# Performance work log

Measured on AMD Instinct MI355X. Metric: run time of the kernel, lower is better.

## Reference

```python
import jax, jax.numpy as jnp
import numpy as np

GROUPS = 8
EPS = 1e-5


def group_norm_dim1(x, gamma, beta):
    # Faithful to torch: GroupNorm treats dim 1 (height) as the channel axis.
    B, H, W, C = x.shape
    xg = x.reshape(B, GROUPS, H // GROUPS, W, C)
    mean = xg.mean(axis=(2, 3, 4), keepdims=True)
    var = xg.var(axis=(2, 3, 4), keepdims=True)
    xn = ((xg - mean) * jax.lax.rsqrt(var + EPS)).reshape(B, H, W, C)
    return xn * gamma[None, :, None, None] + beta[None, :, None, None]


def setup_inputs() -> dict:
    key = jax.random.key(0)
    ks = jax.random.split(key, 8)
    B, H, W, C = 4, 64, 64, 64  # height must equal units for GroupNorm to apply
    s = 1.0 / np.sqrt(C)
    return {
        "x": jax.random.normal(ks[0], (B, H, W, C), dtype=jnp.float32),
        "gamma": jnp.ones((C,), jnp.float32),
        "beta": jnp.zeros((C,), jnp.float32),
        "Wq": jax.random.normal(ks[1], (C, C), jnp.float32) * s,
        "bq": jnp.zeros((C,), jnp.float32),
        "Wk": jax.random.normal(ks[2], (C, C), jnp.float32) * s,
        "bk": jnp.zeros((C,), jnp.float32),
        "Wv": jax.random.normal(ks[3], (C, C), jnp.float32) * s,
        "bv": jnp.zeros((C,), jnp.float32),
        "Wo": jax.random.normal(ks[4], (C, C), jnp.float32) * s,
        "bo": jnp.zeros((C,), jnp.float32),
    }


def reference(x, gamma, beta, Wq, bq, Wk, bk, Wv, bv, Wo, bo):
    B, H, W, C = x.shape
    scale = C ** (-0.5)
    xn = group_norm_dim1(x, gamma, beta)
    q = xn @ Wq + bq
    k = xn @ Wk + bk
    v = xn @ Wv + bv
    # full spatial self-attention: scores [B, H, W, H*W]
    scores = jnp.einsum('bhwc,bijc->bhwij', q, k) * scale
    attn = jax.nn.softmax(scores.reshape(B, H, W, H * W), axis=-1)
    attn = attn.reshape(B, H, W, H, W)
    proj = jnp.einsum('bhwij,bijc->bhwc', attn, v)
    proj = proj @ Wo + bo
    return xn + proj
```

## Files before the change

### kernel.cpp

```cpp
#include <hip/hip_runtime.h>

typedef __bf16 bf16_t;
typedef bf16_t bf16x8 __attribute__((ext_vector_type(8)));
typedef bf16_t bf16x4 __attribute__((ext_vector_type(4)));
typedef short  short4v __attribute__((ext_vector_type(4)));
typedef float  f32x4  __attribute__((ext_vector_type(4)));

#define MFMA32(a, b, c) __builtin_amdgcn_mfma_f32_16x16x32_bf16(a, b, c, 0, 0, 0)
#define MFMA16(a, b, c) __builtin_amdgcn_mfma_f32_16x16x16bf16_1k(a, b, c, 0, 0, 0)

typedef __attribute__((address_space(3))) unsigned int       lds_u32;
typedef __attribute__((address_space(1))) const unsigned int glb_u32c;
#define DMA16(GP, LP) __builtin_amdgcn_global_load_lds((glb_u32c*)(const void*)(GP), \
                                                       (lds_u32*)(void*)(LP), 16, 0, 0)

__global__ __launch_bounds__(256) void gn1w_kernel(const float* __restrict__ x,
    float2* __restrict__ partials,
    const float* __restrict__ Wq, const float* __restrict__ Wk,
    const float* __restrict__ Wv, const float* __restrict__ Wo,
    bf16_t* __restrict__ Wt) {
  int blk = blockIdx.x, t = threadIdx.x;
  if (blk >= 256) {
    int idx = (blk - 256) * 256 + t;
    int wsel = idx >> 12, rem = idx & 4095;
    int c = rem >> 6, kk = rem & 63;
    const float* src = (wsel == 0) ? Wq : ((wsel == 1) ? Wk : ((wsel == 2) ? Wv : Wo));
    Wt[idx] = (bf16_t)src[kk * 64 + c];
    return;
  }
  const float4* x4 = (const float4*)x + (size_t)blk * 1024;
  float s = 0.f, sq = 0.f;
  #pragma unroll
  for (int u = 0; u < 4; ++u) {
    float4 v = x4[u * 256 + t];
    s  += v.x + v.y + v.z + v.w;
    sq += v.x * v.x + v.y * v.y + v.z * v.z + v.w * v.w;
  }
  for (int off = 32; off; off >>= 1) {
    s  += __shfl_down(s, off, 64);
    sq += __shfl_down(sq, off, 64);
  }
  __shared__ float2 ps[4];
  if ((t & 63) == 0) ps[t >> 6] = make_float2(s, sq);
  __syncthreads();
  if (t == 0) {
    float S = 0.f, Q = 0.f;
    #pragma unroll
    for (int i = 0; i < 4; ++i) { S += ps[i].x; Q += ps[i].y; }
    partials[blk] = make_float2(S, Q);
  }
}

__global__ __launch_bounds__(256) void gnqkv_kernel(
    const float* __restrict__ x, const float* __restrict__ gamma,
    const float* __restrict__ beta, const float2* __restrict__ parts,
    const bf16_t* __restrict__ Wt,
    const float* __restrict__ bq, const float* __restrict__ bk, const float* __restrict__ bv,
    bf16_t* __restrict__ xnb, bf16_t* __restrict__ qo, bf16_t* __restrict__ ko,
    bf16_t* __restrict__ vo) {
  __shared__ __align__(16) bf16_t xl[4096];
  int blk = blockIdx.x, t = threadIdx.x;
  int grp = blk >> 3;
  float S = 0.f, Q = 0.f;
  #pragma unroll
  for (int i = 0; i < 8; ++i) { float2 p = parts[grp * 8 + i]; S += p.x; Q += p.y; }
  float mean = S * (1.f / 32768.f);
  float rstd = rsqrtf(Q * (1.f / 32768.f) - mean * mean + 1e-5f);
  int h = blk & 63;
  float ga = gamma[h] * rstd;
  float be = beta[h] - mean * ga;
  {
    int r = t >> 2, col0 = (t & 3) * 16;
    const float4* x4 = (const float4*)(x + (size_t)blk * 4096 + r * 64 + col0);
    bf16x8 pk0, pk1;
    float4 v0 = x4[0], v1 = x4[1], v2 = x4[2], v3 = x4[3];
    pk0[0] = (bf16_t)(v0.x * ga + be); pk0[1] = (bf16_t)(v0.y * ga + be);
    pk0[2] = (bf16_t)(v0.z * ga + be); pk0[3] = (bf16_t)(v0.w * ga + be);
    pk0[4] = (bf16_t)(v1.x * ga + be); pk0[5] = (bf16_t)(v1.y * ga + be);
    pk0[6] = (bf16_t)(v1.z * ga + be); pk0[7] = (bf16_t)(v1.w * ga + be);
    pk1[0] = (bf16_t)(v2.x * ga + be); pk1[1] = (bf16_t)(v2.y * ga + be);
    pk1[2] = (bf16_t)(v2.z * ga + be); pk1[3] = (bf16_t)(v2.w * ga + be);
    pk1[4] = (bf16_t)(v3.x * ga + be); pk1[5] = (bf16_t)(v3.y * ga + be);
    pk1[6] = (bf16_t)(v3.z * ga + be); pk1[7] = (bf16_t)(v3.w * ga + be);
    *(bf16x8*)&xnb[(size_t)blk * 4096 + r * 64 + col0]     = pk0;
    *(bf16x8*)&xnb[(size_t)blk * 4096 + r * 64 + col0 + 8] = pk1;
    int sw = r & 7, j0 = (t & 3) * 2;
    *(bf16x8*)&xl[r * 64 + ((j0 ^ sw) << 3)]       = pk0;
    *(bf16x8*)&xl[r * 64 + (((j0 + 1) ^ sw) << 3)] = pk1;
  }
  __syncthreads();
  int w = t >> 6, lane = t & 63, quad = lane >> 4, l16 = lane & 15;
  int rl = w * 16 + l16, sw2 = rl & 7;
  bf16x8 a0 = *(const bf16x8*)&xl[rl * 64 + ((quad ^ sw2) << 3)];
  bf16x8 a1 = *(const bf16x8*)&xl[rl * 64 + (((quad + 4) ^ sw2) << 3)];
  int m0 = blk * 64 + w * 16;
  int bi = blk >> 6;
  int tile = blk & 63;
  size_t tbase = (size_t)bi * 262144 + (size_t)tile * 4096;
  f32x4 zero = {0.f, 0.f, 0.f, 0.f};
  const float QSCALE = 0.125f * 1.44269504088896340736f;
  #pragma unroll
  for (int outk = 0; outk < 3; ++outk) {
    const bf16_t* wt = Wt + outk * 4096;
    const float* bias = (outk == 0) ? bq : ((outk == 1) ? bk : bv);
    #pragma unroll
    for (int nt = 0; nt < 4; ++nt) {
      int col = nt * 16 + l16;
      bf16x8 b0 = *(const bf16x8*)&wt[col * 64 + quad * 8];
      bf16x8 b1 = *(const bf16x8*)&wt[col * 64 + 32 + quad * 8];
      f32x4 acc = MFMA32(a0, b0, zero);
      acc = MFMA32(a1, b1, acc);
      float bb = bias[col];
      if (outk == 0) {
        #pragma unroll
        for (int r = 0; r < 4; ++r) {
          int m = m0 + quad * 4 + r;
          qo[(size_t)m * 64 + col] = (bf16_t)((acc[r] + bb) * QSCALE);
        }
      } else if (outk == 1) {
        #pragma unroll
        for (int r = 0; r < 4; ++r) {
          int kk = (m0 & 63) + quad * 4 + r;
          ko[tbase + kk * 64 + ((((col >> 3) ^ (kk & 7)) << 3) | (col & 7))]
              = (bf16_t)(acc[r] + bb);
        }
      } else {
        bf16x4 pk;
        #pragma unroll
        for (int r = 0; r < 4; ++r) pk[r] = (bf16_t)(acc[r] + bb);
        int u = w * 4 + quad;
        *(bf16x4*)&vo[tbase + col * 64 + ((u ^ ((col & 7) << 1)) << 2)] = pk;
      }
    }
  }
}

__global__ __launch_bounds__(256, 2) void flash_kernel(
    const bf16_t* __restrict__ q, const bf16_t* __restrict__ k,
    const bf16_t* __restrict__ vp, bf16_t* __restrict__ Opb, float* __restrict__ ml) {
  __shared__ __align__(16) bf16_t Kb[2][8192];
  __shared__ __align__(16) bf16_t Vb[2][8192];
  int t = threadIdx.x;
  int w = t >> 6, lane = t & 63, quad = lane >> 4, l16 = lane & 15;
  int b = blockIdx.x, qb = blockIdx.y, sp = blockIdx.z;
  int q0 = qb * 128 + w * 32;

  bf16x8 qf[2][2];
  {
    const bf16_t* qp = q + ((size_t)b * 4096 + q0 + l16) * 64;
    #pragma unroll
    for (int qt = 0; qt < 2; ++qt)
      #pragma unroll
      for (int hh = 0; hh < 2; ++hh)
        qf[qt][hh] = *(const bf16x8*)&qp[qt * 1024 + hh * 32 + quad * 8];
  }
  f32x4 o[2][4];
  f32x4 zero = {0.f, 0.f, 0.f, 0.f};
  #pragma unroll
  for (int qt = 0; qt < 2; ++qt)
    #pragma unroll
    for (int ct = 0; ct < 4; ++ct) o[qt][ct] = zero;
  float rs[2] = {0.f, 0.f};

  const bf16_t* kimg = k  + (size_t)b * 262144 + (size_t)sp * 65536 + w * 2048 + lane * 8;
  const bf16_t* vimg = vp + (size_t)b * 262144 + (size_t)sp * 65536 + w * 2048 + lane * 8;

  #pragma unroll
  for (int i = 0; i < 4; ++i) {
    DMA16(kimg + i * 512, &Kb[0][w * 2048 + i * 512]);
    DMA16(vimg + i * 512, &Vb[0][w * 2048 + i * 512]);
  }
  __syncthreads();

  int swk = l16 & 7;
  int swv = (l16 & 7) << 1;

  for (int it = 0; it < 8; ++it) {
    int cur = it & 1;
    if (it < 7) {
      const bf16_t* kg = kimg + (it + 1) * 8192;
      const bf16_t* vg = vimg + (it + 1) * 8192;
      int nxt = cur ^ 1;
      #pragma unroll
      for (int i = 0; i < 4; ++i) {
        DMA16(kg + i * 512, &Kb[nxt][w * 2048 + i * 512]);
        DMA16(vg + i * 512, &Vb[nxt][w * 2048 + i * 512]);
      }
    }
    #pragma unroll
    for (int kt = 0; kt < 8; ++kt) {
      const bf16_t* Kh = &Kb[cur][(kt >> 2) * 4096];
      const bf16_t* Vh = &Vb[cur][(kt >> 2) * 4096];
      int krow = ((kt & 3) * 16 + l16) * 64;
      bf16x8 kf0 = *(const bf16x8*)&Kh[krow + ((quad ^ swk) << 3)];
      bf16x8 kf1 = *(const bf16x8*)&Kh[krow + (((quad + 4) ^ swk) << 3)];
      short4v va[4];
      #pragma unroll
      for (int ct = 0; ct < 4; ++ct)
        va[ct] = *(const short4v*)&Vh[(ct * 16 + l16) * 64 + ((((kt & 3) * 4 + quad) ^ swv) << 2)];
      #pragma unroll
      for (int qt = 0; qt < 2; ++qt) {
        f32x4 st = MFMA32(kf0, qf[qt][0], zero);
        st = MFMA32(kf1, qf[qt][1], st);
        bf16x4 pb;
        float psum = 0.f;
        #pragma unroll
        for (int r = 0; r < 4; ++r) {
          float p = __builtin_amdgcn_exp2f(st[r]);
          psum += p;
          pb[r] = (bf16_t)p;
        }
        rs[qt] += psum;
        short4v pshort = __builtin_bit_cast(short4v, pb);
        #pragma unroll
        for (int ct = 0; ct < 4; ++ct)
          o[qt][ct] = MFMA16(va[ct], pshort, o[qt][ct]);
      }
    }
    __syncthreads();
  }

  #pragma unroll
  for (int qt = 0; qt < 2; ++qt) {
    rs[qt] += __shfl_xor(rs[qt], 16, 64);
    rs[qt] += __shfl_xor(rs[qt], 32, 64);
  }
  size_t rbase = (size_t)sp * 16384 + (size_t)b * 4096 + q0;
  #pragma unroll
  for (int qt = 0; qt < 2; ++qt) {
    size_t row = rbase + qt * 16 + l16;
    if (quad == 0) ml[row] = rs[qt];
    #pragma unroll
    for (int ct = 0; ct < 4; ++ct) {
      bf16x4 pk;
      #pragma unroll
      for (int r = 0; r < 4; ++r) pk[r] = (bf16_t)o[qt][ct][r];
      *(bf16x4*)&Opb[row * 64 + ct * 16 + quad * 4] = pk;
    }
  }
}

__global__ __launch_bounds__(256) void proj_kernel(
    const bf16_t* __restrict__ Opb, const float* __restrict__ ml,
    const bf16_t* __restrict__ Wt, const float* __restrict__ bo,
    const bf16_t* __restrict__ xnb, float* __restrict__ out) {
  int t = threadIdx.x, w = t >> 6, lane = t & 63, quad = lane >> 4, l16 = lane & 15;
  int r0 = blockIdx.x * 64 + w * 16;
  float acc0[8], acc1[8];
  #pragma unroll
  for (int e = 0; e < 8; ++e) { acc0[e] = 0.f; acc1[e] = 0.f; }
  float lsum = 0.f;
  #pragma unroll
  for (int s = 0; s < 4; ++s) {
    size_t rr = (size_t)s * 16384 + r0 + l16;
    bf16x8 f0 = *(const bf16x8*)&Opb[rr * 64 + quad * 8];
    bf16x8 f1 = *(const bf16x8*)&Opb[rr * 64 + 32 + quad * 8];
    #pragma unroll
    for (int e = 0; e < 8; ++e) { acc0[e] += (float)f0[e]; acc1[e] += (float)f1[e]; }
    lsum += ml[rr];
  }
  float linv = 1.f / lsum;
  bf16x8 a0, a1;
  #pragma unroll
  for (int e = 0; e < 8; ++e) {
    a0[e] = (bf16_t)(acc0[e] * linv);
    a1[e] = (bf16_t)(acc1[e] * linv);
  }
  f32x4 zero = {0.f, 0.f, 0.f, 0.f};
  const bf16_t* wt = Wt + 3 * 4096;
  #pragma unroll
  for (int nt = 0; nt < 4; ++nt) {
    int col = nt * 16 + l16;
    bf16x8 b0 = *(const bf16x8*)&wt[col * 64 + quad * 8];
    bf16x8 b1 = *(const bf16x8*)&wt[col * 64 + 32 + quad * 8];
    f32x4 acc = MFMA32(a0, b0, zero);
    acc = MFMA32(a1, b1, acc);
    float bb = bo[col];
    #pragma unroll
    for (int r = 0; r < 4; ++r) {
      size_t m = (size_t)r0 + quad * 4 + r;
      out[m * 64 + col] = acc[r] + bb + (float)xnb[m * 64 + col];
    }
  }
}

extern "C" void kernel_launch(void* const* d_in, const int* in_sizes, int n_in,
                              void* d_out, int out_size, void* d_ws, size_t ws_size,
                              hipStream_t stream) {
  const float* x     = (const float*)d_in[0];
  const float* gamma = (const float*)d_in[1];
  const float* beta  = (const float*)d_in[2];
  const float* Wq    = (const float*)d_in[3];
  const float* bq    = (const float*)d_in[4];
  const float* Wk    = (const float*)d_in[5];
  const float* bk    = (const float*)d_in[6];
  const float* Wv    = (const float*)d_in[7];
  const float* bv    = (const float*)d_in[8];
  const float* Wo    = (const float*)d_in[9];
  const float* bo    = (const float*)d_in[10];
  float* out = (float*)d_out;

  char* ws = (char*)d_ws;
  bf16_t* xnb   = (bf16_t*)(ws + 0);
  bf16_t* qb    = (bf16_t*)(ws + (2u  << 20));
  bf16_t* kb    = (bf16_t*)(ws + (4u  << 20));
  bf16_t* vb    = (bf16_t*)(ws + (6u  << 20));
  bf16_t* Opb   = (bf16_t*)(ws + (8u  << 20));
  float*  ml    = (float*)(ws + (16u << 20));
  float2* parts = (float2*)(ws + (17u << 20));
  bf16_t* Wt    = (bf16_t*)(ws + (17u << 20) + 4096);

  hipLaunchKernelGGL(gn1w_kernel,  dim3(320),       dim3(256), 0, stream, x, parts, Wq, Wk, Wv, Wo, Wt);
  hipLaunchKernelGGL(gnqkv_kernel, dim3(256),       dim3(256), 0, stream, x, gamma, beta, parts, Wt, bq, bk, bv, xnb, qb, kb, vb);
  hipLaunchKernelGGL(flash_kernel, dim3(4, 32, 4),  dim3(256), 0, stream, qb, kb, vb, Opb, ml);
  hipLaunchKernelGGL(proj_kernel,  dim3(256),       dim3(256), 0, stream, Opb, ml, Wt, bo, xnb, out);
}
```

Baseline: 120.6 us.

## Stage QKV outputs through LDS for coalesced stores and widen V reads

The projection kernel now writes each Q and K tile into shared memory first, then copies it to global memory with contiguous 16-byte stores instead of scattered 2-byte writes. The V image layout is changed to an 8-element swizzle, which the attention kernel reads with 16-byte loads covering two key subtiles. The attention loop is reorganised so one wide V load feeds two MFMA steps. This aims to cut uncoalesced global stores and halve LDS read instructions for V, at the cost of extra barriers in the projection kernel and a layout change that both kernels must agree on.

```diff
diff --git a/kernel.cpp b/kernel.cpp
--- a/kernel.cpp
+++ b/kernel.cpp
@@ -4,6 +4,7 @@
 typedef bf16_t bf16x8 __attribute__((ext_vector_type(8)));
 typedef bf16_t bf16x4 __attribute__((ext_vector_type(4)));
 typedef short  short4v __attribute__((ext_vector_type(4)));
+typedef short  short8v __attribute__((ext_vector_type(8)));
 typedef float  f32x4  __attribute__((ext_vector_type(4)));
 
 #define MFMA32(a, b, c) __builtin_amdgcn_mfma_f32_16x16x32_bf16(a, b, c, 0, 0, 0)
@@ -93,45 +94,62 @@
   int rl = w * 16 + l16, sw2 = rl & 7;
   bf16x8 a0 = *(const bf16x8*)&xl[rl * 64 + ((quad ^ sw2) << 3)];
   bf16x8 a1 = *(const bf16x8*)&xl[rl * 64 + (((quad + 4) ^ sw2) << 3)];
+  __syncthreads();
   int m0 = blk * 64 + w * 16;
   int bi = blk >> 6;
   int tile = blk & 63;
   size_t tbase = (size_t)bi * 262144 + (size_t)tile * 4096;
   f32x4 zero = {0.f, 0.f, 0.f, 0.f};
   const float QSCALE = 0.125f * 1.44269504088896340736f;
-  #pragma unroll
-  for (int outk = 0; outk < 3; ++outk) {
-    const bf16_t* wt = Wt + outk * 4096;
-    const float* bias = (outk == 0) ? bq : ((outk == 1) ? bk : bv);
-    #pragma unroll
-    for (int nt = 0; nt < 4; ++nt) {
-      int col = nt * 16 + l16;
-      bf16x8 b0 = *(const bf16x8*)&wt[col * 64 + quad * 8];
-      bf16x8 b1 = *(const bf16x8*)&wt[col * 64 + 32 + quad * 8];
-      f32x4 acc = MFMA32(a0, b0, zero);
-      acc = MFMA32(a1, b1, acc);
-      float bb = bias[col];
-      if (outk == 0) {
-        #pragma unroll
-        for (int r = 0; r < 4; ++r) {
-          int m = m0 + quad * 4 + r;
-          qo[(size_t)m * 64 + col] = (bf16_t)((acc[r] + bb) * QSCALE);
-        }
-      } else if (outk == 1) {
-        #pragma unroll
-        for (int r = 0; r < 4; ++r) {
-          int kk = (m0 & 63) + quad * 4 + r;
-          ko[tbase + kk * 64 + ((((col >> 3) ^ (kk & 7)) << 3) | (col & 7))]
-              = (bf16_t)(acc[r] + bb);
-        }
-      } else {
-        bf16x4 pk;
-        #pragma unroll
-        for (int r = 0; r < 4; ++r) pk[r] = (bf16_t)(acc[r] + bb);
-        int u = w * 4 + quad;
-        *(bf16x4*)&vo[tbase + col * 64 + ((u ^ ((col & 7) << 1)) << 2)] = pk;
-      }
-    }
+
+  #pragma unroll
+  for (int nt = 0; nt < 4; ++nt) {
+    int col = nt * 16 + l16;
+    bf16x8 b0 = *(const bf16x8*)&Wt[col * 64 + quad * 8];
+    bf16x8 b1 = *(const bf16x8*)&Wt[col * 64 + 32 + quad * 8];
+    f32x4 acc = MFMA32(a0, b0, zero);
+    acc = MFMA32(a1, b1, acc);
+    float bb = bq[col];
+    #pragma unroll
+    for (int r = 0; r < 4; ++r)
+      xl[(w * 16 + quad * 4 + r) * 64 + col] = (bf16_t)((acc[r] + bb) * QSCALE);
+  }
+  __syncthreads();
+  *(bf16x8*)&qo[(size_t)blk * 4096 + t * 16]     = *(const bf16x8*)&xl[t * 16];
+  *(bf16x8*)&qo[(size_t)blk * 4096 + t * 16 + 8] = *(const bf16x8*)&xl[t * 16 + 8];
+  __syncthreads();
+
+  #pragma unroll
+  for (int nt = 0; nt < 4; ++nt) {
+    int col = nt * 16 + l16;
+    bf16x8 b0 = *(const bf16x8*)&Wt[4096 + col * 64 + quad * 8];
+    bf16x8 b1 = *(const bf16x8*)&Wt[4096 + col * 64 + 32 + quad * 8];
+    f32x4 acc = MFMA32(a0, b0, zero);
+    acc = MFMA32(a1, b1, acc);
+    float bb = bk[col];
+    #pragma unroll
+    for (int r = 0; r < 4; ++r) {
+      int kk = w * 16 + quad * 4 + r;
+      xl[kk * 64 + ((((col >> 3) ^ (kk & 7)) << 3) | (col & 7))] = (bf16_t)(acc[r] + bb);
+    }
+  }
+  __syncthreads();
+  *(bf16x8*)&ko[tbase + t * 16]     = *(const bf16x8*)&xl[t * 16];
+  *(bf16x8*)&ko[tbase + t * 16 + 8] = *(const bf16x8*)&xl[t * 16 + 8];
+
+  #pragma unroll
+  for (int nt = 0; nt < 4; ++nt) {
+    int col = nt * 16 + l16;
+    bf16x8 b0 = *(const bf16x8*)&Wt[8192 + col * 64 + quad * 8];
+    bf16x8 b1 = *(const bf16x8*)&Wt[8192 + col * 64 + 32 + quad * 8];
+    f32x4 acc = MFMA32(a0, b0, zero);
+    acc = MFMA32(a1, b1, acc);
+    float bb = bv[col];
+    bf16x4 pk;
+    #pragma unroll
+    for (int r = 0; r < 4; ++r) pk[r] = (bf16_t)(acc[r] + bb);
+    int ch = (w >> 1) * 4 + quad;
+    *(bf16x4*)&vo[tbase + (size_t)col * 64 + ((ch ^ (col & 7)) << 3) + (w & 1) * 4] = pk;
   }
 }
 
@@ -173,7 +191,7 @@
   __syncthreads();
 
   int swk = l16 & 7;
-  int swv = (l16 & 7) << 1;
+  int swv = l16 & 7;
 
   for (int it = 0; it < 8; ++it) {
     int cur = it & 1;
@@ -188,33 +206,43 @@
       }
     }
     #pragma unroll
-    for (int kt = 0; kt < 8; ++kt) {
-      const bf16_t* Kh = &Kb[cur][(kt >> 2) * 4096];
-      const bf16_t* Vh = &Vb[cur][(kt >> 2) * 4096];
-      int krow = ((kt & 3) * 16 + l16) * 64;
-      bf16x8 kf0 = *(const bf16x8*)&Kh[krow + ((quad ^ swk) << 3)];
-      bf16x8 kf1 = *(const bf16x8*)&Kh[krow + (((quad + 4) ^ swk) << 3)];
-      short4v va[4];
+    for (int hh = 0; hh < 2; ++hh) {
+      const bf16_t* Kh = &Kb[cur][hh * 4096];
+      const bf16_t* Vh = &Vb[cur][hh * 4096];
       #pragma unroll
-      for (int ct = 0; ct < 4; ++ct)
-        va[ct] = *(const short4v*)&Vh[(ct * 16 + l16) * 64 + ((((kt & 3) * 4 + quad) ^ swv) << 2)];
-      #pragma unroll
-      for (int qt = 0; qt < 2; ++qt) {
-        f32x4 st = MFMA32(kf0, qf[qt][0], zero);
-        st = MFMA32(kf1, qf[qt][1], st);
-        bf16x4 pb;
-        float psum = 0.f;
-        #pragma unroll
-        for (int r = 0; r < 4; ++r) {
-          float p = __builtin_amdgcn_exp2f(st[r]);
-          psum += p;
-          pb[r] = (bf16_t)p;
-        }
-        rs[qt] += psum;
-        short4v pshort = __builtin_bit_cast(short4v, pb);
+      for (int m = 0; m < 2; ++m) {
+        short8v vp8[4];
         #pragma unroll
         for (int ct = 0; ct < 4; ++ct)
-          o[qt][ct] = MFMA16(va[ct], pshort, o[qt][ct]);
+          vp8[ct] = *(const short8v*)&Vh[(ct * 16 + l16) * 64 + (((m * 4 + quad) ^ swv) << 3)];
+        #pragma unroll
+        for (int k2 = 0; k2 < 2; ++k2) {
+          int ktl = m * 2 + k2;
+          int krow = (ktl * 16 + l16) * 64;
+          bf16x8 kf0 = *(const bf16x8*)&Kh[krow + ((quad ^ swk) << 3)];
+          bf16x8 kf1 = *(const bf16x8*)&Kh[krow + (((quad + 4) ^ swk) << 3)];
+          #pragma unroll
+          for (int qt = 0; qt < 2; ++qt) {
+            f32x4 st = MFMA32(kf0, qf[qt][0], zero);
+            st = MFMA32(kf1, qf[qt][1], st);
+            bf16x4 pb;
+            float psum = 0.f;
+            #pragma unroll
+            for (int r = 0; r < 4; ++r) {
+              float p = __builtin_amdgcn_exp2f(st[r]);
+              psum += p;
+              pb[r] = (bf16_t)p;
+            }
+            rs[qt] += psum;
+            short4v pshort = __builtin_bit_cast(short4v, pb);
+            #pragma unroll
+            for (int ct = 0; ct < 4; ++ct) {
+              short4v va = k2 ? __builtin_shufflevector(vp8[ct], vp8[ct], 4, 5, 6, 7)
+                              : __builtin_shufflevector(vp8[ct], vp8[ct], 0, 1, 2, 3);
+              o[qt][ct] = MFMA16(va, pshort, o[qt][ct]);
+            }
+          }
+        }
       }
     }
     __syncthreads();
```

Measured after the change: 121.8 us. Within noise of the previous version (+1.0%).
